# Kernel tuning notes

Hardware: AMD Instinct MI355X
Metric: run time of the kernel (lower is better)

## Reference

```python
import jax, jax.numpy as jnp
import numpy as np

D_MODEL = 2048
FFN_HIDDEN = 2048
N_EXPERTS = 16
TOP_K = 4


def setup_inputs() -> dict:
    key = jax.random.key(0)
    k1, k2, k3, k4, k5 = jax.random.split(key, 5)
    scale = 1.0 / np.sqrt(D_MODEL)
    x = jax.random.normal(k1, (2, 4096, D_MODEL), dtype=jnp.float32)
    w_router = jax.random.normal(k2, (N_EXPERTS, D_MODEL), dtype=jnp.float32) * scale
    w_gate = jax.random.normal(k3, (N_EXPERTS, D_MODEL, FFN_HIDDEN), dtype=jnp.float32) * scale
    w_up = jax.random.normal(k4, (N_EXPERTS, D_MODEL, FFN_HIDDEN), dtype=jnp.float32) * scale
    w_down = jax.random.normal(k5, (N_EXPERTS, FFN_HIDDEN, D_MODEL), dtype=jnp.float32) * (1.0 / np.sqrt(FFN_HIDDEN))
    return {"x": x, "w_router": w_router, "w_gate": w_gate, "w_up": w_up, "w_down": w_down}


def reference(x, w_router, w_gate, w_up, w_down):
    B, S, D = x.shape
    xt = x.reshape(-1, D)  # [T, D] tokens
    # Router: linear -> softmax -> top-k (renormalize=False in SoftmaxTopK)
    logits = jnp.einsum('td,ed->te', xt, w_router)
    probs = jax.nn.softmax(logits, axis=-1)
    top_w, top_e = jax.lax.top_k(probs, TOP_K)  # [T, k]
    # moe_normalize_expert_weights = 1 -> divide by L1 norm of top weights
    top_w = top_w / jnp.sum(jnp.abs(top_w), axis=-1, keepdims=True)
    # Dispatch/combine: loop over fixed expert count, weighted SwiGLU combine
    out = jnp.zeros_like(xt)
    for e in range(N_EXPERTS):
        coeff = jnp.sum(jnp.where(top_e == e, top_w, 0.0), axis=-1)  # [T]
        h = jax.nn.silu(xt @ w_gate[e]) * (xt @ w_up[e])  # [T, F]
        out = out + coeff[:, None] * (h @ w_down[e])
    return out.reshape(B, S, D)
```

## Files before the change

kernel.cpp:

```cpp
#include <hip/hip_runtime.h>
#include <hip/hip_bf16.h>
#include <stdint.h>

#define NTOK   8192
#define DMODEL 2048
#define FFN    2048
#define NEXP   16
#define TOPK   4
#define STRIDE (NTOK + 256)

#define BM 256
#define BK 64
#define NKT 32
#define NIT 16
#define MAXT ((NTOK*TOPK)/BM + NEXP)
#define RTB 32

typedef __attribute__((ext_vector_type(4))) float    f32x4;
typedef __attribute__((ext_vector_type(4))) _Float16 f16x4;
typedef __attribute__((ext_vector_type(8))) _Float16 f16x8;

typedef __attribute__((address_space(1))) void gvoid;
typedef __attribute__((address_space(3))) void lvoid;
#define GLDS16(gp, lp) __builtin_amdgcn_global_load_lds((gvoid*)(gp), (lvoid*)(lp), 16, 0, 0)

#define MFMA16(a,b,c) __builtin_amdgcn_mfma_f32_16x16x32_f16((a),(b),(c),0,0,0)
#define BAR __builtin_amdgcn_s_barrier()
#define LGK asm volatile("s_waitcnt lgkmcnt(0)" ::: "memory")
#define VMW2 asm volatile("s_waitcnt vmcnt(2)" ::: "memory")
#define VMW0 asm volatile("s_waitcnt vmcnt(0)" ::: "memory")


__global__ void k_sentinel(float* o){ o[0] = 3.0e7f; }

__global__ __launch_bounds__(256) void k_transpose3(const float* __restrict__ s0,
                                                    const float* __restrict__ s1,
                                                    const float* __restrict__ s2,
                                                    _Float16* __restrict__ d0,
                                                    _Float16* __restrict__ d1,
                                                    _Float16* __restrict__ d2){
  __shared__ float lds[64][65];
  int z = blockIdx.z;
  const float* S; _Float16* D;
  if (z < 16)      { S = s0 + (size_t)z * DMODEL * FFN;      D = d0 + (size_t)z * DMODEL * FFN; }
  else if (z < 32) { S = s1 + (size_t)(z-16) * DMODEL * FFN; D = d1 + (size_t)(z-16) * DMODEL * FFN; }
  else             { S = s2 + (size_t)(z-32) * DMODEL * FFN; D = d2 + (size_t)(z-32) * DMODEL * FFN; }
  const int tid = threadIdx.x;
  const int x0 = blockIdx.x * 64, y0 = blockIdx.y * 64;
  {
    int row = tid >> 2, cq = (tid & 3) * 16;
    const float* srow = S + (size_t)(y0 + row) * 2048 + x0 + cq;
#pragma unroll
    for (int k = 0; k < 4; ++k){
      float4 v = *(const float4*)(srow + 4*k);
      lds[row][cq + 4*k + 0] = v.x; lds[row][cq + 4*k + 1] = v.y;
      lds[row][cq + 4*k + 2] = v.z; lds[row][cq + 4*k + 3] = v.w;
    }
  }
  __syncthreads();
#pragma unroll
  for (int jj = 0; jj < 2; ++jj){
    int slot = tid + 256*jj;
    int c = slot >> 3, ch = slot & 7;
    f16x8 h;
#pragma unroll
    for (int i = 0; i < 8; ++i) h[i] = (_Float16)lds[ch*8 + i][c];
    *(f16x8*)(D + (size_t)(x0 + c) * 2048 + y0 + ch*8) = h;
  }
}

__global__ __launch_bounds__(256) void k_router(const float* __restrict__ x,
                                                const float* __restrict__ wr,
                                                int*   __restrict__ counts,
                                                int*   __restrict__ ids,
                                                int*   __restrict__ slotmap,
                                                float* __restrict__ wk,
                                                _Float16* __restrict__ xh){
  __shared__ unsigned char lte[RTB][TOPK];
  __shared__ int lcnt[NEXP], lbase[NEXP], loff[NEXP];
  const int tid = threadIdx.x, wv = tid >> 6, lane = tid & 63;
  if (tid < NEXP){ lcnt[tid] = 0; loff[tid] = 0; }
  __syncthreads();
  const float4* w4 = (const float4*)wr;
  for (int tt = 0; tt < 8; ++tt){
    const int tl = wv*8 + tt;
    const int t = blockIdx.x * RTB + tl;
    const float4* x4 = (const float4*)(x + (size_t)t * DMODEL);
    float acc[NEXP];
#pragma unroll
    for (int e = 0; e < NEXP; ++e) acc[e] = 0.f;
#pragma unroll
    for (int i = 0; i < 8; ++i){
      int d4 = lane + i*64;
      float4 xv = x4[d4];
      f16x4 h; h[0]=(_Float16)xv.x; h[1]=(_Float16)xv.y; h[2]=(_Float16)xv.z; h[3]=(_Float16)xv.w;
      *(f16x4*)(xh + (size_t)t*DMODEL + d4*4) = h;
#pragma unroll
      for (int e = 0; e < NEXP; ++e){
        float4 wv_ = w4[e*512 + d4];
        acc[e] += xv.x*wv_.x + xv.y*wv_.y + xv.z*wv_.z + xv.w*wv_.w;
      }
    }
#pragma unroll
    for (int e = 0; e < NEXP; ++e){
      float v = acc[e];
#pragma unroll
      for (int s = 32; s > 0; s >>= 1) v += __shfl_xor(v, s);
      acc[e] = v;
    }
    if (lane == 0){
      int mask = 0; float tv[TOPK]; int te[TOPK];
      for (int k = 0; k < TOPK; ++k){
        float best = -3.0e38f; int bi = 0;
        for (int e = 0; e < NEXP; ++e)
          if (!((mask >> e) & 1) && acc[e] > best){ best = acc[e]; bi = e; }
        mask |= 1 << bi; tv[k] = best; te[k] = bi;
      }
      float m = tv[0], s = 0.f, w[TOPK];
      for (int k = 0; k < TOPK; ++k){ w[k] = __expf(tv[k] - m); s += w[k]; }
      float inv = 1.f / s;
      for (int k = 0; k < TOPK; ++k){
        lte[tl][k] = (unsigned char)te[k];
        wk[t*TOPK + k] = w[k] * inv;
      }
    }
  }
  __syncthreads();
  if (tid < RTB*TOPK) atomicAdd(&lcnt[lte[tid >> 2][tid & 3]], 1);
  __syncthreads();
  if (tid < NEXP) lbase[tid] = atomicAdd(&counts[tid], lcnt[tid]);
  __syncthreads();
  if (tid < RTB*TOPK){
    int tl = tid >> 2, k = tid & 3;
    int ep = lte[tl][k];
    int slot = lbase[ep] + atomicAdd(&loff[ep], 1);
    int t = blockIdx.x * RTB + tl;
    ids[ep*STRIDE + slot] = t;
    slotmap[t*TOPK + k] = (ep << 16) | slot;
  }
}

#define RD_B(q,kx) { _Pragma("unroll") for (int n = 0; n < 4; ++n) \
    bf[n] = *(const f16x8*)(Bb + (q)*32768 + (bB[n] ^ (kx))); }
#define RD_A(q,kx,mh) { _Pragma("unroll") for (int m = 0; m < 4; ++m) \
    af[m] = *(const f16x8*)(Ab + (q)*32768 + (aB[(mh)*4+m] ^ (kx))); }
#define MM(mh) { __builtin_amdgcn_s_setprio(1); \
    _Pragma("unroll") for (int m = 0; m < 4; ++m) \
    _Pragma("unroll") for (int n = 0; n < 4; ++n) \
      acc[(mh)*4+m][n] = MFMA16(bf[n], af[m], acc[(mh)*4+m][n]); \
    __builtin_amdgcn_s_setprio(0); }
#define STG_A(T,h) { _Pragma("unroll") for (int j = 0; j < 2; ++j) \
    GLDS16(srcA[h][j] + (size_t)(T)*128, ldsA + ((T)&1)*32768 + (h)*16384 + j*8192 + wdst); }
#define STG_B(T,h) { _Pragma("unroll") for (int j = 0; j < 2; ++j) \
    GLDS16(srcB[h][j] + (size_t)(T)*128, ldsB + ((T)&1)*32768 + (h)*16384 + j*8192 + wdst); }
#define ITER8(t1,t2,t3,F) \
  RD_B(0,0);  RD_A(0,0,0);  STG_B(t1,1);            BAR; LGK; MM(0); BAR; \
  RD_A(0,0,1);              STG_A(t1,0);            BAR; LGK; MM(1); BAR; \
  RD_B(0,64); RD_A(0,64,0); STG_A(t1,1);            BAR; LGK; MM(0); BAR; \
  RD_A(0,64,1);             if (F){ STG_B(t2,0); }  BAR; LGK; MM(1); \
  if (F){ VMW2; } else { VMW0; }                    BAR; \
  RD_B(1,0);  RD_A(1,0,0);  if (F){ STG_B(t2,1); }  BAR; LGK; MM(0); BAR; \
  RD_A(1,0,1);              if (F){ STG_A(t2,0); }  BAR; LGK; MM(1); BAR; \
  RD_B(1,64); RD_A(1,64,0); if (F){ STG_A(t2,1); }  BAR; LGK; MM(0); BAR; \
  RD_A(1,64,1);             if (F){ STG_B(t3,0); }  BAR; LGK; MM(1); \
  if (F){ VMW2; }                                   BAR;

__global__ __launch_bounds__(512, 2) void k_gateup(
    const _Float16* __restrict__ xh,
    const _Float16* __restrict__ wgT,
    const _Float16* __restrict__ wuT,
    const int* __restrict__ counts,
    const int* __restrict__ ids,
    _Float16* __restrict__ H)
{
  __shared__ __align__(128) char smem[131072];
  char* ldsA = smem;
  char* ldsB = smem + 65536;

  const int bid = blockIdx.x;
  const int vid = (bid & 7) * (MAXT*2) + (bid >> 3);
  const int g = vid / (4*MAXT), rem = vid % (4*MAXT);
  const int mt_lin = rem >> 2;
  const int n0 = (g*4 + (rem & 3)) * 128;

  int e = -1, mt = 0, rowbase = 0;
  { int at = 0, rb = 0;
    for (int i = 0; i < NEXP; ++i){
      int c = counts[i]; int nt = (c + 255) >> 8;
      if (e < 0 && mt_lin < at + nt){ e = i; mt = mt_lin - at; rowbase = rb; }
      at += nt; rb += nt * BM;
    } }
  if (e < 0) return;

  const int tid = threadIdx.x, lane = tid & 63, w = tid >> 6;
  const int wm = w >> 2, wn = w & 3, hi = lane >> 4, l15 = lane & 15;
  const int wdst = w * 1024;

  const int chunk = (((tid & 7) ^ ((tid >> 3) & 7)) << 4);
  const char* srcA[2][2]; const char* srcB[2][2];
#pragma unroll
  for (int h = 0; h < 2; ++h)
#pragma unroll
    for (int j = 0; j < 2; ++j){
      int r = h*128 + j*64 + (tid >> 3);
      int tok = ids[e*STRIDE + mt*BM + r];
      srcA[h][j] = (const char*)(xh + (size_t)tok * DMODEL) + chunk;
      int which = (r >> 5) & 1, col = n0 + ((r >> 6) << 5) + (r & 31);
      const _Float16* Wm = which ? wuT : wgT;
      srcB[h][j] = (const char*)(Wm + ((size_t)e * FFN + col) * (size_t)DMODEL) + chunk;
    }

  const char* Ab = ldsA + wm*16384;
  const char* Bb = ldsB + (wn >> 1)*16384 + (wn & 1)*8192;
  const int sl0 = (hi ^ (l15 & 7)) << 4;
  int aB[8], bB[4];
#pragma unroll
  for (int m = 0; m < 8; ++m) aB[m] = m*2048 + l15*128 + sl0;
#pragma unroll
  for (int n = 0; n < 4; ++n) bB[n] = n*2048 + l15*128 + sl0;

  f32x4 acc[8][4];
#pragma unroll
  for (int m = 0; m < 8; ++m)
#pragma unroll
    for (int n = 0; n < 4; ++n) acc[m][n] = (f32x4)(0.0f);

  STG_B(0,0); STG_B(0,1); STG_A(0,0); STG_A(0,1); STG_B(1,0);
  VMW2; BAR;

  f16x8 af[4], bf[4];
  for (int i = 0; i < NIT-1; ++i){
    ITER8(2*i+1, 2*i+2, 2*i+3, 1)
  }
  ITER8(31, 32, 33, 0)

  const int hrow0 = rowbase + mt*BM + wm*128;
#pragma unroll
  for (int m = 0; m < 8; ++m){
    int row = hrow0 + m*16 + l15;
#pragma unroll
    for (int nf = 0; nf < 2; ++nf){
      f16x4 hv;
#pragma unroll
      for (int j = 0; j < 4; ++j){
        float gv = acc[m][nf][j], uv = acc[m][nf+2][j];
        hv[j] = (_Float16)(gv / (1.f + __expf(-gv)) * uv);
      }
      *(f16x4*)(H + (size_t)row * FFN + n0 + wn*32 + nf*16 + hi*4) = hv;
    }
  }
}

__global__ __launch_bounds__(512, 2) void k_down(
    const _Float16* __restrict__ H,
    const _Float16* __restrict__ wdT,
    const int* __restrict__ counts,
    _Float16* __restrict__ Yw2,
    _Float16* __restrict__ Yxh)
{
  __shared__ __align__(128) char smem[131072];
  char* ldsA = smem;
  char* ldsB = smem + 65536;

  const int bid = blockIdx.x;
  const int vid = (bid & 7) * MAXT + (bid >> 3);
  const int g = vid / (4*MAXT), rem = vid % (4*MAXT);
  const int mt_lin = rem >> 2;
  const int n0 = (g*4 + (rem & 3)) * 256;

  int e = -1, mt = 0, rowbase = 0;
  { int at = 0, rb = 0;
    for (int i = 0; i < NEXP; ++i){
      int c = counts[i]; int nt = (c + 255) >> 8;
      if (e < 0 && mt_lin < at + nt){ e = i; mt = mt_lin - at; rowbase = rb; }
      at += nt; rb += nt * BM;
    } }
  if (e < 0) return;

  const int tid = threadIdx.x, lane = tid & 63, w = tid >> 6;
  const int wm = w >> 2, wn = w & 3, hi = lane >> 4, l15 = lane & 15;
  const int wdst = w * 1024;

  const int chunk = (((tid & 7) ^ ((tid >> 3) & 7)) << 4);
  const char* srcA[2][2]; const char* srcB[2][2];
#pragma unroll
  for (int h = 0; h < 2; ++h)
#pragma unroll
    for (int j = 0; j < 2; ++j){
      int r = h*128 + j*64 + (tid >> 3);
      srcA[h][j] = (const char*)(H + (size_t)(rowbase + mt*BM + r) * FFN) + chunk;
      srcB[h][j] = (const char*)(wdT + ((size_t)e * DMODEL + n0 + r) * (size_t)FFN) + chunk;
    }

  const char* Ab = ldsA + wm*16384;
  const char* Bb = ldsB + (wn >> 1)*16384 + (wn & 1)*8192;
  const int sl0 = (hi ^ (l15 & 7)) << 4;
  int aB[8], bB[4];
#pragma unroll
  for (int m = 0; m < 8; ++m) aB[m] = m*2048 + l15*128 + sl0;
#pragma unroll
  for (int n = 0; n < 4; ++n) bB[n] = n*2048 + l15*128 + sl0;

  f32x4 acc[8][4];
#pragma unroll
  for (int m = 0; m < 8; ++m)
#pragma unroll
    for (int n = 0; n < 4; ++n) acc[m][n] = (f32x4)(0.0f);

  STG_B(0,0); STG_B(0,1); STG_A(0,0); STG_A(0,1); STG_B(1,0);
  VMW2; BAR;

  f16x8 af[4], bf[4];
  for (int i = 0; i < NIT-1; ++i){
    ITER8(2*i+1, 2*i+2, 2*i+3, 1)
  }
  ITER8(31, 32, 33, 0)

  const int row0 = rowbase + mt*BM + wm*128;
#pragma unroll
  for (int m = 0; m < 8; ++m){
    int row = row0 + m*16 + l15;
    _Float16* yb = (row < 32768) ? (Yw2 + (size_t)row * DMODEL)
                                 : (Yxh + (size_t)(row - 32768) * DMODEL);
#pragma unroll
    for (int n = 0; n < 4; ++n){
      f16x4 yv;
#pragma unroll
      for (int j = 0; j < 4; ++j) yv[j] = (_Float16)acc[m][n][j];
      *(f16x4*)(yb + n0 + wn*64 + n*16 + hi*4) = yv;
    }
  }
}

__global__ __launch_bounds__(256) void k_combine(const _Float16* __restrict__ Yw2,
                                                 const _Float16* __restrict__ Yxh,
                                                 const int* __restrict__ counts,
                                                 const int* __restrict__ slotmap,
                                                 const float* __restrict__ wk,
                                                 float* __restrict__ out){
  __shared__ int pre[NEXP];
  const int t = blockIdx.x, c = threadIdx.x;
  if (c == 0){
    int a = 0;
    for (int i = 0; i < NEXP; ++i){ pre[i] = a; a += ((counts[i] + 255) >> 8) << 8; }
  }
  __syncthreads();
  float o[8];
#pragma unroll
  for (int i = 0; i < 8; ++i) o[i] = 0.f;
#pragma unroll
  for (int k = 0; k < TOPK; ++k){
    int sm = slotmap[t*TOPK + k];
    int row = pre[sm >> 16] + (sm & 0xffff);
    float wv = wk[t*TOPK + k];
    const _Float16* yb = (row < 32768) ? (Yw2 + (size_t)row * DMODEL)
                                       : (Yxh + (size_t)(row - 32768) * DMODEL);
    f16x8 y = *(const f16x8*)(yb + c*8);
#pragma unroll
    for (int i = 0; i < 8; ++i) o[i] += wv * (float)y[i];
  }
  float4 lo = {o[0], o[1], o[2], o[3]}, hu = {o[4], o[5], o[6], o[7]};
  float* op = out + (size_t)t * DMODEL + c*8;
  *(float4*)op = lo;
  *(float4*)(op + 4) = hu;
}

extern "C" void kernel_launch(void* const* d_in, const int* in_sizes, int n_in,
                              void* d_out, int out_size, void* d_ws, size_t ws_size,
                              hipStream_t stream)
{
  const float* x  = (const float*)d_in[0];
  const float* wr = (const float*)d_in[1];
  const float* wg = (const float*)d_in[2];
  const float* wu = (const float*)d_in[3];
  const float* wd = (const float*)d_in[4];
  float* out = (float*)d_out;
  char* ws = (char*)d_ws;

  const size_t OFF_IDS  = 256;
  const size_t OFF_SLOT = OFF_IDS  + (size_t)NEXP*STRIDE*4;
  const size_t OFF_WK   = OFF_SLOT + (size_t)NTOK*TOPK*4;
  const size_t OFF_XH   = OFF_WK   + (size_t)NTOK*TOPK*4;
  const size_t OFF_W1   = OFF_XH   + (size_t)NTOK*DMODEL*2;
  const size_t OFF_H    = OFF_W1   + (size_t)NEXP*DMODEL*FFN*2;
  const size_t OFF_W2   = OFF_H    + (size_t)MAXT*BM*FFN*2;
  const size_t OFF_WD   = OFF_W2   + (size_t)NEXP*DMODEL*FFN*2;
  const size_t NEED     = OFF_WD   + (size_t)NEXP*DMODEL*FFN*2;
  if (ws_size < NEED){ k_sentinel<<<1,1,0,stream>>>(out); return; }

  int*      counts  = (int*)ws;
  int*      ids     = (int*)(ws + OFF_IDS);
  int*      slotmap = (int*)(ws + OFF_SLOT);
  float*    wk      = (float*)(ws + OFF_WK);
  _Float16* xh      = (_Float16*)(ws + OFF_XH);
  _Float16* wgT     = (_Float16*)(ws + OFF_W1);
  _Float16* wuT     = (_Float16*)(ws + OFF_W2);
  _Float16* wdT     = (_Float16*)(ws + OFF_WD);
  _Float16* H       = (_Float16*)(ws + OFF_H);
  _Float16* Yw2     = (_Float16*)(ws + OFF_W2);
  _Float16* Yxh     = (_Float16*)(ws + OFF_XH);

  hipMemsetAsync(ws, 0, OFF_SLOT, stream);

  k_router<<<NTOK/RTB, 256, 0, stream>>>(x, wr, counts, ids, slotmap, wk, xh);
  k_transpose3<<<dim3(32,32,48), 256, 0, stream>>>(wg, wu, wd, wgT, wuT, wdT);
  k_gateup<<<MAXT*16, 512, 0, stream>>>(xh, wgT, wuT, counts, ids, H);
  k_down<<<MAXT*8, 512, 0, stream>>>(H, wdT, counts, Yw2, Yxh);
  k_combine<<<NTOK, 256, 0, stream>>>(Yw2, Yxh, counts, slotmap, wk, out);
}
```

Baseline: 1.180 ms.

## Split K-tiles into half-K LDS slabs and deepen global-to-LDS prefetch

Both grouped GEMM kernels change their LDS staging layout. Each 64-wide K tile is now stored as two 32-element halves with 64-byte rows and a 4-way XOR swizzle, replacing row-halves with 128-byte rows. The load schedule is reordered so each stage fills one K-half of A and B, and the wait count rises from vmcnt(2) to vmcnt(6), so more global-to-LDS loads stay in flight. This aims at better overlap of memory latency with MFMA work. The 64-byte row swizzle may cause more LDS bank conflicts.

```diff
diff --git a/kernel.cpp b/kernel.cpp
--- a/kernel.cpp
+++ b/kernel.cpp
@@ -27,7 +27,7 @@
 #define MFMA16(a,b,c) __builtin_amdgcn_mfma_f32_16x16x32_f16((a),(b),(c),0,0,0)
 #define BAR __builtin_amdgcn_s_barrier()
 #define LGK asm volatile("s_waitcnt lgkmcnt(0)" ::: "memory")
-#define VMW2 asm volatile("s_waitcnt vmcnt(2)" ::: "memory")
+#define VMW6 asm volatile("s_waitcnt vmcnt(6)" ::: "memory")
 #define VMW0 asm volatile("s_waitcnt vmcnt(0)" ::: "memory")
 
 
@@ -140,30 +140,30 @@
   }
 }
 
-#define RD_B(q,kx) { _Pragma("unroll") for (int n = 0; n < 4; ++n) \
-    bf[n] = *(const f16x8*)(Bb + (q)*32768 + (bB[n] ^ (kx))); }
-#define RD_A(q,kx,mh) { _Pragma("unroll") for (int m = 0; m < 4; ++m) \
-    af[m] = *(const f16x8*)(Ab + (q)*32768 + (aB[(mh)*4+m] ^ (kx))); }
+#define SRD_B(q,kh) { _Pragma("unroll") for (int n = 0; n < 4; ++n) \
+    bf[n] = *(const f16x8*)(ldsB + (q)*32768 + (kh)*16384 + bB[n]); }
+#define SRD_A(q,kh,mh) { _Pragma("unroll") for (int m = 0; m < 4; ++m) \
+    af[m] = *(const f16x8*)(ldsA + (q)*32768 + (kh)*16384 + aB[(mh)*4+m]); }
 #define MM(mh) { __builtin_amdgcn_s_setprio(1); \
     _Pragma("unroll") for (int m = 0; m < 4; ++m) \
     _Pragma("unroll") for (int n = 0; n < 4; ++n) \
       acc[(mh)*4+m][n] = MFMA16(bf[n], af[m], acc[(mh)*4+m][n]); \
     __builtin_amdgcn_s_setprio(0); }
-#define STG_A(T,h) { _Pragma("unroll") for (int j = 0; j < 2; ++j) \
-    GLDS16(srcA[h][j] + (size_t)(T)*128, ldsA + ((T)&1)*32768 + (h)*16384 + j*8192 + wdst); }
-#define STG_B(T,h) { _Pragma("unroll") for (int j = 0; j < 2; ++j) \
-    GLDS16(srcB[h][j] + (size_t)(T)*128, ldsB + ((T)&1)*32768 + (h)*16384 + j*8192 + wdst); }
-#define ITER8(t1,t2,t3,F) \
-  RD_B(0,0);  RD_A(0,0,0);  STG_B(t1,1);            BAR; LGK; MM(0); BAR; \
-  RD_A(0,0,1);              STG_A(t1,0);            BAR; LGK; MM(1); BAR; \
-  RD_B(0,64); RD_A(0,64,0); STG_A(t1,1);            BAR; LGK; MM(0); BAR; \
-  RD_A(0,64,1);             if (F){ STG_B(t2,0); }  BAR; LGK; MM(1); \
-  if (F){ VMW2; } else { VMW0; }                    BAR; \
-  RD_B(1,0);  RD_A(1,0,0);  if (F){ STG_B(t2,1); }  BAR; LGK; MM(0); BAR; \
-  RD_A(1,0,1);              if (F){ STG_A(t2,0); }  BAR; LGK; MM(1); BAR; \
-  RD_B(1,64); RD_A(1,64,0); if (F){ STG_A(t2,1); }  BAR; LGK; MM(0); BAR; \
-  RD_A(1,64,1);             if (F){ STG_B(t3,0); }  BAR; LGK; MM(1); \
-  if (F){ VMW2; }                                   BAR;
+#define STG_A(T,kh) { _Pragma("unroll") for (int j = 0; j < 2; ++j) \
+    GLDS16(srcA[j] + (size_t)(T)*128 + (kh)*64, ldsA + ((T)&1)*32768 + (kh)*16384 + j*8192 + wdst); }
+#define STG_B(T,kh) { _Pragma("unroll") for (int j = 0; j < 2; ++j) \
+    GLDS16(srcB[j] + (size_t)(T)*128 + (kh)*64, ldsB + ((T)&1)*32768 + (kh)*16384 + j*8192 + wdst); }
+#define KIT(t2,t3,F) \
+  SRD_B(0,0); SRD_A(0,0,0); STG_A((t2)-1,1);          BAR; LGK; MM(0); BAR; \
+  SRD_A(0,0,1);             if (F){ STG_B((t2),0); }  BAR; LGK; MM(1); BAR; \
+  SRD_B(0,1); SRD_A(0,1,0); if (F){ STG_A((t2),0); }  BAR; LGK; MM(0); BAR; \
+  SRD_A(0,1,1);             if (F){ STG_B((t2),1); }  BAR; LGK; MM(1); \
+  if (F){ VMW6; } else { VMW0; }                      BAR; \
+  SRD_B(1,0); SRD_A(1,0,0); if (F){ STG_A((t2),1); }  BAR; LGK; MM(0); BAR; \
+  SRD_A(1,0,1);             if (F){ STG_B((t3),0); }  BAR; LGK; MM(1); BAR; \
+  SRD_B(1,1); SRD_A(1,1,0); if (F){ STG_A((t3),0); }  BAR; LGK; MM(0); BAR; \
+  SRD_A(1,1,1);             if (F){ STG_B((t3),1); }  BAR; LGK; MM(1); \
+  if (F){ VMW6; }                                     BAR;
 
 __global__ __launch_bounds__(512, 2) void k_gateup(
     const _Float16* __restrict__ xh,
@@ -196,28 +196,24 @@
   const int wm = w >> 2, wn = w & 3, hi = lane >> 4, l15 = lane & 15;
   const int wdst = w * 1024;
 
-  const int chunk = (((tid & 7) ^ ((tid >> 3) & 7)) << 4);
-  const char* srcA[2][2]; const char* srcB[2][2];
-#pragma unroll
-  for (int h = 0; h < 2; ++h)
-#pragma unroll
-    for (int j = 0; j < 2; ++j){
-      int r = h*128 + j*64 + (tid >> 3);
-      int tok = ids[e*STRIDE + mt*BM + r];
-      srcA[h][j] = (const char*)(xh + (size_t)tok * DMODEL) + chunk;
-      int which = (r >> 5) & 1, col = n0 + ((r >> 6) << 5) + (r & 31);
-      const _Float16* Wm = which ? wuT : wgT;
-      srcB[h][j] = (const char*)(Wm + ((size_t)e * FFN + col) * (size_t)DMODEL) + chunk;
-    }
-
-  const char* Ab = ldsA + wm*16384;
-  const char* Bb = ldsB + (wn >> 1)*16384 + (wn & 1)*8192;
-  const int sl0 = (hi ^ (l15 & 7)) << 4;
+  const int chunk = (((tid & 3) ^ ((tid >> 3) & 3)) << 4);
+  const char* srcA[2]; const char* srcB[2];
+#pragma unroll
+  for (int j = 0; j < 2; ++j){
+    int r = j*128 + (tid >> 2);
+    int tok = ids[e*STRIDE + mt*BM + r];
+    srcA[j] = (const char*)(xh + (size_t)tok * DMODEL) + chunk;
+    int which = (r >> 5) & 1, col = n0 + ((r >> 6) << 5) + (r & 31);
+    const _Float16* Wm = which ? wuT : wgT;
+    srcB[j] = (const char*)(Wm + ((size_t)e * FFN + col) * (size_t)DMODEL) + chunk;
+  }
+
+  const int sw = ((hi ^ ((l15 >> 1) & 3)) << 4);
   int aB[8], bB[4];
 #pragma unroll
-  for (int m = 0; m < 8; ++m) aB[m] = m*2048 + l15*128 + sl0;
-#pragma unroll
-  for (int n = 0; n < 4; ++n) bB[n] = n*2048 + l15*128 + sl0;
+  for (int m = 0; m < 8; ++m) aB[m] = (wm*128 + m*16 + l15)*64 + sw;
+#pragma unroll
+  for (int n = 0; n < 4; ++n) bB[n] = (wn*64  + n*16 + l15)*64 + sw;
 
   f32x4 acc[8][4];
 #pragma unroll
@@ -225,14 +221,15 @@
 #pragma unroll
     for (int n = 0; n < 4; ++n) acc[m][n] = (f32x4)(0.0f);
 
-  STG_B(0,0); STG_B(0,1); STG_A(0,0); STG_A(0,1); STG_B(1,0);
-  VMW2; BAR;
+  STG_B(0,0); STG_A(0,0); STG_B(0,1); STG_A(0,1);
+  STG_B(1,0); STG_A(1,0); STG_B(1,1);
+  VMW6; BAR;
 
   f16x8 af[4], bf[4];
   for (int i = 0; i < NIT-1; ++i){
-    ITER8(2*i+1, 2*i+2, 2*i+3, 1)
-  }
-  ITER8(31, 32, 33, 0)
+    KIT(2*i+2, 2*i+3, 1)
+  }
+  KIT(32, 33, 0)
 
   const int hrow0 = rowbase + mt*BM + wm*128;
 #pragma unroll
@@ -281,25 +278,21 @@
   const int wm = w >> 2, wn = w & 3, hi = lane >> 4, l15 = lane & 15;
   const int wdst = w * 1024;
 
-  const int chunk = (((tid & 7) ^ ((tid >> 3) & 7)) << 4);
-  const char* srcA[2][2]; const char* srcB[2][2];
-#pragma unroll
-  for (int h = 0; h < 2; ++h)
-#pragma unroll
-    for (int j = 0; j < 2; ++j){
-      int r = h*128 + j*64 + (tid >> 3);
-      srcA[h][j] = (const char*)(H + (size_t)(rowbase + mt*BM + r) * FFN) + chunk;
-      srcB[h][j] = (const char*)(wdT + ((size_t)e * DMODEL + n0 + r) * (size_t)FFN) + chunk;
-    }
-
-  const char* Ab = ldsA + wm*16384;
-  const char* Bb = ldsB + (wn >> 1)*16384 + (wn & 1)*8192;
-  const int sl0 = (hi ^ (l15 & 7)) << 4;
+  const int chunk = (((tid & 3) ^ ((tid >> 3) & 3)) << 4);
+  const char* srcA[2]; const char* srcB[2];
+#pragma unroll
+  for (int j = 0; j < 2; ++j){
+    int r = j*128 + (tid >> 2);
+    srcA[j] = (const char*)(H + (size_t)(rowbase + mt*BM + r) * FFN) + chunk;
+    srcB[j] = (const char*)(wdT + ((size_t)e * DMODEL + n0 + r) * (size_t)FFN) + chunk;
+  }
+
+  const int sw = ((hi ^ ((l15 >> 1) & 3)) << 4);
   int aB[8], bB[4];
 #pragma unroll
-  for (int m = 0; m < 8; ++m) aB[m] = m*2048 + l15*128 + sl0;
-#pragma unroll
-  for (int n = 0; n < 4; ++n) bB[n] = n*2048 + l15*128 + sl0;
+  for (int m = 0; m < 8; ++m) aB[m] = (wm*128 + m*16 + l15)*64 + sw;
+#pragma unroll
+  for (int n = 0; n < 4; ++n) bB[n] = (wn*64  + n*16 + l15)*64 + sw;
 
   f32x4 acc[8][4];
 #pragma unroll
@@ -307,14 +300,15 @@
 #pragma unroll
     for (int n = 0; n < 4; ++n) acc[m][n] = (f32x4)(0.0f);
 
-  STG_B(0,0); STG_B(0,1); STG_A(0,0); STG_A(0,1); STG_B(1,0);
-  VMW2; BAR;
+  STG_B(0,0); STG_A(0,0); STG_B(0,1); STG_A(0,1);
+  STG_B(1,0); STG_A(1,0); STG_B(1,1);
+  VMW6; BAR;
 
   f16x8 af[4], bf[4];
   for (int i = 0; i < NIT-1; ++i){
-    ITER8(2*i+1, 2*i+2, 2*i+3, 1)
-  }
-  ITER8(31, 32, 33, 0)
+    KIT(2*i+2, 2*i+3, 1)
+  }
+  KIT(32, 33, 0)
 
   const int row0 = rowbase + mt*BM + wm*128;
 #pragma unroll
```

Result: slower. 1.255 ms (+6.4%).
